# Kernel tuning notes

Hardware: AMD Instinct MI355X
Metric: run time of the kernel (lower is better)

Reference implementation:

```python
import math
import jax, jax.numpy as jnp
import numpy as np

B, T, D = 2, 1024, 512
H, DK = 8, 64


def setup_inputs() -> dict:
    key = jax.random.key(0)
    ks = jax.random.split(key, 7)
    s = 1.0 / math.sqrt(D)
    x = jax.random.normal(ks[0], (B, T, D), dtype=jnp.float32)
    Wq = jax.random.normal(ks[1], (D, H * DK), dtype=jnp.float32) * s
    Wk = jax.random.normal(ks[2], (D, H * DK), dtype=jnp.float32) * s
    Wv = jax.random.normal(ks[3], (D, H * DK), dtype=jnp.float32) * s
    Wo = jax.random.normal(ks[4], (H * DK, D), dtype=jnp.float32) * s
    Wg = jax.random.normal(ks[5], (D, H * DK), dtype=jnp.float32) * 0.02
    bg = jnp.ones((H * DK,), dtype=jnp.float32)  # gate_bias_init = 1.0
    return {"x": x, "Wq": Wq, "Wk": Wk, "Wv": Wv, "Wo": Wo, "Wg": Wg, "bg": bg}


def reference(x, Wq, Wk, Wv, Wo, Wg, bg):
    b, t, d = x.shape
    Q = jax.nn.relu(x @ Wq).reshape(b, t, H, DK)
    K = jax.nn.relu(x @ Wk).reshape(b, t, H, DK)
    V = (x @ Wv).reshape(b, t, H, DK)
    angle = jnp.arange(t, dtype=x.dtype) * (math.pi / (2 * t))  # (T,)
    cosw = jnp.cos(angle)[None, :, None, None]
    sinw = jnp.sin(angle)[None, :, None, None]
    Qc, Qs = Q * cosw, Q * sinw
    Kc, Ks = K * cosw, K * sinw
    # cumulative KV outer products: (B,T,H,DK,DK)
    Sc = jnp.cumsum(jnp.einsum('bthd,bthe->bthde', Kc, V), axis=1)
    Ss = jnp.cumsum(jnp.einsum('bthd,bthe->bthde', Ks, V), axis=1)
    o = jnp.einsum('bthd,bthde->bthe', Qc, Sc) + jnp.einsum('bthd,bthde->bthe', Qs, Ss)
    zc = jnp.cumsum(Kc, axis=1)
    zs = jnp.cumsum(Ks, axis=1)
    z = jnp.einsum('bthd,bthd->bth', Qc, zc) + jnp.einsum('bthd,bthd->bth', Qs, zs)
    z = jnp.maximum(z, 1e-6)[..., None]
    o = o / z
    gate = jax.nn.sigmoid((x @ Wg + bg).reshape(b, t, H, DK))
    o = o * gate
    return o.reshape(b, t, H * DK) @ Wo
```

## Files before the change

kernel.cpp:

```cpp
#include <hip/hip_runtime.h>
#include <math.h>

#define B_ 2
#define T_ 1024
#define D_ 512
#define H_ 8
#define DK_ 64
#define NBH_ 16
#define C_ 32
#define G_ 32

#define PI_OVER_2T 0.00153398078788564122971808758949f

typedef float f32x4 __attribute__((ext_vector_type(4)));
typedef short s16x8 __attribute__((ext_vector_type(8)));

__device__ __forceinline__ ushort f2bf(float x) {
    unsigned u = __float_as_uint(x);
    unsigned r = (u + 0x7fffu + ((u >> 16) & 1u)) >> 16;
    return (ushort)r;
}
__device__ __forceinline__ float bf2f(ushort u) {
    return __uint_as_float((unsigned)u << 16);
}

__device__ __forceinline__ void async16(void* lds, const void* g) {
    __builtin_amdgcn_global_load_lds(
        (const __attribute__((address_space(1))) void*)g,
        (__attribute__((address_space(3))) void*)lds, 16, 0, 0);
}

__global__ __launch_bounds__(256) void k_conv(
    const float* __restrict__ x,
    const float* __restrict__ Wq, const float* __restrict__ Wk,
    const float* __restrict__ Wv, const float* __restrict__ Wg,
    const float* __restrict__ Wo,
    ushort* __restrict__ xb, ushort* __restrict__ WtAll)
{
    __shared__ float Ts[64][65];
    const int bx = blockIdx.x;
    const int tid = threadIdx.x;
    if (bx < 1024) {
        int i = (bx * 256 + tid) * 4;
        float4 v = *(const float4*)&x[i];
        ushort4 o;
        o.x = f2bf(v.x); o.y = f2bf(v.y); o.z = f2bf(v.z); o.w = f2bf(v.w);
        *(ushort4*)&xb[i] = o;
        return;
    }
    const int bid = bx - 1024;
    const int mi = bid >> 6;
    const int t64 = bid & 63;
    const float* __restrict__ W = (mi == 0) ? Wq : (mi == 1) ? Wk
                                 : (mi == 2) ? Wv : (mi == 3) ? Wg : Wo;
    const int tr = t64 >> 3, tc = t64 & 7;
#pragma unroll
    for (int p = 0; p < 4; p++) {
        int row = p * 16 + (tid >> 4);
        int c4 = (tid & 15) * 4;
        float4 v = *(const float4*)&W[(size_t)(tr * 64 + row) * 512 + tc * 64 + c4];
        Ts[row][c4 + 0] = v.x; Ts[row][c4 + 1] = v.y;
        Ts[row][c4 + 2] = v.z; Ts[row][c4 + 3] = v.w;
    }
    __syncthreads();
    const int nl = tid >> 2, kc = (tid & 3) * 16;
    ushort buf[16];
#pragma unroll
    for (int u = 0; u < 16; u++) buf[u] = f2bf(Ts[kc + u][nl]);
    ushort* dst = WtAll + (size_t)mi * 262144 + (size_t)(tc * 64 + nl) * 512
                  + tr * 64 + kc;
    *(uint4*)dst = *(uint4*)&buf[0];
    *(uint4*)(dst + 8) = *(uint4*)&buf[8];
}

__global__ __launch_bounds__(256) void k_g0(
    const ushort* __restrict__ A, const ushort* __restrict__ WtAll,
    const float* __restrict__ bg,
    ushort* __restrict__ Qg, ushort* __restrict__ Kg,
    ushort* __restrict__ Vg, ushort* __restrict__ Gg,
    ushort* __restrict__ Sst, float* __restrict__ Zst)
{
    __shared__ union {
        struct { ushort As[2][64 * 64]; ushort Bs[2][2 * 64 * 64]; } s;
        struct { ushort KcT[64 * 72]; ushort KsT[64 * 72];
                 ushort VT[64 * 72]; ushort KR[64 * 72];
                 ushort VR[64 * 72]; } e;
    } sm;
    __shared__ float cosR[64], sinR[64];

    const int tid = threadIdx.x;
    const int ct = blockIdx.x;
    const int rowBase = blockIdx.y * 64;
    const bool isKV = (ct >= 8);
    const int matCol = (ct & 7) * 64;
    const ushort* __restrict__ B0 = WtAll + (size_t)(isKV ? 1 : 0) * 262144;
    const ushort* __restrict__ B1 = WtAll + (size_t)(isKV ? 2 : 3) * 262144;

    const int wave = tid >> 6, lane = tid & 63;
    const int q = lane >> 4, ln = lane & 15;
    const int mB = (wave >> 1) * 32, nB = (wave & 1) * 32;

    int fu[2];
    const ushort* gA[2];
    const ushort* gB0[2];
    const ushort* gB1[2];
#pragma unroll
    for (int u = 0; u < 2; u++) {
        int f = tid * 8 + u * 2048;
        int r = f >> 6;
        int gc = ((f >> 3) & 7) ^ (r & 7);
        fu[u] = f;
        gA[u]  = A  + (size_t)(rowBase + r) * 512 + gc * 8;
        gB0[u] = B0 + (size_t)(matCol + r) * 512 + gc * 8;
        gB1[u] = B1 + (size_t)(matCol + r) * 512 + gc * 8;
    }

    f32x4 accA[2][2], accB[2][2];
#pragma unroll
    for (int i = 0; i < 2; i++)
#pragma unroll
        for (int j = 0; j < 2; j++) {
            accA[i][j] = (f32x4){0.f, 0.f, 0.f, 0.f};
            accB[i][j] = (f32x4){0.f, 0.f, 0.f, 0.f};
        }

    int aoff[2][2], boff[2][2];
#pragma unroll
    for (int i = 0; i < 2; i++) {
        int ra = mB + i * 16 + ln;
#pragma unroll
        for (int ks = 0; ks < 2; ks++)
            aoff[i][ks] = ra * 64 + (((ks * 4 + q) ^ (ra & 7)) * 8);
    }
#pragma unroll
    for (int j = 0; j < 2; j++) {
        int rb = nB + j * 16 + ln;
#pragma unroll
        for (int ks = 0; ks < 2; ks++)
            boff[j][ks] = rb * 64 + (((ks * 4 + q) ^ (rb & 7)) * 8);
    }

#pragma unroll
    for (int u = 0; u < 2; u++) {
        async16(&sm.s.As[0][fu[u]], gA[u]);
        async16(&sm.s.Bs[0][fu[u]], gB0[u]);
        async16(&sm.s.Bs[0][4096 + fu[u]], gB1[u]);
    }

    int cur = 0;
    for (int kb = 0; kb < 512; kb += 64) {
        __syncthreads();
        if (kb + 64 < 512) {
            int nxt = cur ^ 1;
#pragma unroll
            for (int u = 0; u < 2; u++) {
                async16(&sm.s.As[nxt][fu[u]], gA[u] + kb + 64);
                async16(&sm.s.Bs[nxt][fu[u]], gB0[u] + kb + 64);
                async16(&sm.s.Bs[nxt][4096 + fu[u]], gB1[u] + kb + 64);
            }
        }
#pragma unroll
        for (int ks = 0; ks < 2; ks++) {
            s16x8 af[2], b0f[2], b1f[2];
#pragma unroll
            for (int i = 0; i < 2; i++)
                af[i] = *(const s16x8*)&sm.s.As[cur][aoff[i][ks]];
#pragma unroll
            for (int j = 0; j < 2; j++) {
                b0f[j] = *(const s16x8*)&sm.s.Bs[cur][boff[j][ks]];
                b1f[j] = *(const s16x8*)&sm.s.Bs[cur][4096 + boff[j][ks]];
            }
#pragma unroll
            for (int i = 0; i < 2; i++)
#pragma unroll
                for (int j = 0; j < 2; j++) {
                    accA[i][j] = __builtin_amdgcn_mfma_f32_16x16x32_bf16(
                        af[i], b0f[j], accA[i][j], 0, 0, 0);
                    accB[i][j] = __builtin_amdgcn_mfma_f32_16x16x32_bf16(
                        af[i], b1f[j], accB[i][j], 0, 0, 0);
                }
        }
        cur ^= 1;
    }
    if (isKV && tid < 64) {
        float a = (float)((rowBase + tid) & 1023) * PI_OVER_2T;
        cosR[tid] = cosf(a);
        sinR[tid] = sinf(a);
    }
    __syncthreads();

    if (!isKV) {
        ushort* QT = sm.e.KcT;
        ushort* GT = sm.e.KsT;
#pragma unroll
        for (int i = 0; i < 2; i++)
#pragma unroll
            for (int j = 0; j < 2; j++) {
                int colL = nB + j * 16 + ln;
                float bgv = bg[matCol + colL];
#pragma unroll
                for (int r = 0; r < 4; r++) {
                    int rowL = mB + i * 16 + q * 4 + r;
                    QT[rowL * 72 + colL] = f2bf(fmaxf(accA[i][j][r], 0.f));
                    GT[rowL * 72 + colL] =
                        f2bf(1.f / (1.f + expf(-(accB[i][j][r] + bgv))));
                }
            }
        __syncthreads();
#pragma unroll
        for (int it = 0; it < 2; it++) {
            int row = it * 32 + (tid >> 3), sub = tid & 7;
            uint4 qv = *(const uint4*)&QT[row * 72 + sub * 8];
            uint4 gv = *(const uint4*)&GT[row * 72 + sub * 8];
            size_t go = (size_t)(rowBase + row) * 512 + matCol + sub * 8;
            *(uint4*)&Qg[go] = qv;
            *(uint4*)&Gg[go] = gv;
        }
        return;
    }

    const int h = ct - 8;
    const int b = rowBase >> 10;
    const int c = wave >> 1;
    const int gG = ((rowBase & 1023) >> 5) + c;
    const int blk = (b * 8 + h) * 32 + gG;

    float zc[2] = {0.f, 0.f}, zs[2] = {0.f, 0.f};
#pragma unroll
    for (int i = 0; i < 2; i++)
#pragma unroll
        for (int r = 0; r < 4; r++) {
            int tLoc = mB + i * 16 + q * 4 + r;
            float ca = cosR[tLoc], sa = sinR[tLoc];
#pragma unroll
            for (int j = 0; j < 2; j++) {
                int col = nB + j * 16 + ln;
                float kv = fmaxf(accA[i][j][r], 0.f);
                float vv = accB[i][j][r];
                sm.e.KR[tLoc * 72 + col] = f2bf(kv);
                sm.e.VR[tLoc * 72 + col] = f2bf(vv);
                float kc = kv * ca, ks = kv * sa;
                sm.e.KcT[col * 72 + tLoc] = f2bf(kc);
                sm.e.KsT[col * 72 + tLoc] = f2bf(ks);
                sm.e.VT [col * 72 + tLoc] = f2bf(vv);
                zc[j] += kc; zs[j] += ks;
            }
        }
#pragma unroll
    for (int j = 0; j < 2; j++) {
        zc[j] += __shfl_xor(zc[j], 16); zc[j] += __shfl_xor(zc[j], 32);
        zs[j] += __shfl_xor(zs[j], 16); zs[j] += __shfl_xor(zs[j], 32);
    }
    if (q == 0) {
#pragma unroll
        for (int j = 0; j < 2; j++) {
            int d = nB + j * 16 + ln;
            Zst[(size_t)blk * 128 + d] = zc[j];
            Zst[(size_t)blk * 128 + 64 + d] = zs[j];
        }
    }
    __syncthreads();

#pragma unroll
    for (int it = 0; it < 2; it++) {
        int row = it * 32 + (tid >> 3), sub = tid & 7;
        uint4 kv4 = *(const uint4*)&sm.e.KR[row * 72 + sub * 8];
        uint4 vv4 = *(const uint4*)&sm.e.VR[row * 72 + sub * 8];
        size_t go = (size_t)(rowBase + row) * 512 + h * 64 + sub * 8;
        *(uint4*)&Kg[go] = kv4;
        *(uint4*)&Vg[go] = vv4;
    }

    {
        const int eh = (wave & 1) * 32;
        ushort* Sp = Sst + (size_t)blk * 8192;
        s16x8 av[2];
#pragma unroll
        for (int fi = 0; fi < 2; fi++)
            av[fi] = *(const s16x8*)&sm.e.VT[(eh + fi * 16 + ln) * 72
                                            + c * 32 + q * 8];
#pragma unroll
        for (int fj = 0; fj < 4; fj++) {
            s16x8 bc = *(const s16x8*)&sm.e.KcT[(fj * 16 + ln) * 72
                                                + c * 32 + q * 8];
            s16x8 bs = *(const s16x8*)&sm.e.KsT[(fj * 16 + ln) * 72
                                                + c * 32 + q * 8];
#pragma unroll
            for (int fi = 0; fi < 2; fi++) {
                f32x4 sc = __builtin_amdgcn_mfma_f32_16x16x32_bf16(
                    av[fi], bc, (f32x4){0.f, 0.f, 0.f, 0.f}, 0, 0, 0);
                f32x4 ss = __builtin_amdgcn_mfma_f32_16x16x32_bf16(
                    av[fi], bs, (f32x4){0.f, 0.f, 0.f, 0.f}, 0, 0, 0);
#pragma unroll
                for (int rr = 0; rr < 4; rr++) {
                    int e = eh + fi * 16 + q * 4 + rr;
                    int d = fj * 16 + ln;
                    Sp[e * 64 + d] = f2bf(sc[rr]);
                    Sp[4096 + e * 64 + d] = f2bf(ss[rr]);
                }
            }
        }
    }
}

template<int MODE, int TM, int TN, int BK>
__global__ __launch_bounds__(256) void k_gemm(
    const ushort* __restrict__ A, const ushort* __restrict__ Bt,
    const float* __restrict__ bg,
    void* __restrict__ O0v, void* __restrict__ O1v,
    void* __restrict__ O2v, void* __restrict__ O3v)
{
    constexpr int WM = TM / 2, WN = TN / 2;
    constexpr int FM = WM / 16, FN = WN / 16;
    constexpr int CH = BK / 8;
    constexpr int SH = (BK == 32) ? 1 : 0;
    constexpr int KS = BK / 32;
    constexpr int NA = TM * BK / 2048;
    constexpr int NB = TN * BK / 2048;
    static_assert(TM == 64 && TN == 32, "epilogue specialized");

    __shared__ ushort As[2][TM * BK];
    __shared__ ushort Bs[2][TN * BK];

    const int tid = threadIdx.x;
    const int ct = blockIdx.x;
    const int rowBase = blockIdx.y * TM;

    const int matCol = ct * TN;
    const ushort* __restrict__ Bmat = Bt;

    const int wave = tid >> 6, lane = tid & 63;
    const int q = lane >> 4, ln = lane & 15;
    const int mB = (wave >> 1) * WM, nB = (wave & 1) * WN;

    int fuA[NA], fuB[NB];
    const ushort* gA[NA];
    const ushort* gB[NB];
#pragma unroll
    for (int u = 0; u < NA; u++) {
        int fu = tid * 8 + u * 2048;
        int r = fu / BK;
        int slot = (fu >> 3) & (CH - 1);
        int gc = slot ^ ((r >> SH) & (CH - 1));
        fuA[u] = fu;
        gA[u] = A + (size_t)(rowBase + r) * 512 + gc * 8;
    }
#pragma unroll
    for (int u = 0; u < NB; u++) {
        int fu = tid * 8 + u * 2048;
        int r = fu / BK;
        int slot = (fu >> 3) & (CH - 1);
        int gc = slot ^ ((r >> SH) & (CH - 1));
        fuB[u] = fu;
        gB[u] = Bmat + (size_t)(matCol + r) * 512 + gc * 8;
    }

    f32x4 acc[FM][FN];
#pragma unroll
    for (int i = 0; i < FM; i++)
#pragma unroll
        for (int j = 0; j < FN; j++) acc[i][j] = (f32x4){0.f, 0.f, 0.f, 0.f};

    int aoff[FM][KS], boff[FN][KS];
#pragma unroll
    for (int i = 0; i < FM; i++) {
        int ra = mB + i * 16 + ln;
#pragma unroll
        for (int ks = 0; ks < KS; ks++)
            aoff[i][ks] = ra * BK + (((ks * 4 + q) ^ ((ra >> SH) & (CH - 1))) * 8);
    }
#pragma unroll
    for (int j = 0; j < FN; j++) {
        int rb = nB + j * 16 + ln;
#pragma unroll
        for (int ks = 0; ks < KS; ks++)
            boff[j][ks] = rb * BK + (((ks * 4 + q) ^ ((rb >> SH) & (CH - 1))) * 8);
    }

#pragma unroll
    for (int u = 0; u < NA; u++) async16(&As[0][fuA[u]], gA[u]);
#pragma unroll
    for (int u = 0; u < NB; u++) async16(&Bs[0][fuB[u]], gB[u]);

    int cur = 0;
    for (int kb = 0; kb < 512; kb += BK) {
        __syncthreads();
        if (kb + BK < 512) {
#pragma unroll
            for (int u = 0; u < NA; u++)
                async16(&As[cur ^ 1][fuA[u]], gA[u] + kb + BK);
#pragma unroll
            for (int u = 0; u < NB; u++)
                async16(&Bs[cur ^ 1][fuB[u]], gB[u] + kb + BK);
        }
#pragma unroll
        for (int ks = 0; ks < KS; ks++) {
            s16x8 af[FM], bf[FN];
#pragma unroll
            for (int i = 0; i < FM; i++)
                af[i] = *(const s16x8*)&As[cur][aoff[i][ks]];
#pragma unroll
            for (int j = 0; j < FN; j++)
                bf[j] = *(const s16x8*)&Bs[cur][boff[j][ks]];
#pragma unroll
            for (int i = 0; i < FM; i++)
#pragma unroll
                for (int j = 0; j < FN; j++)
                    acc[i][j] = __builtin_amdgcn_mfma_f32_16x16x32_bf16(
                        af[i], bf[j], acc[i][j], 0, 0, 0);
        }
        cur ^= 1;
    }
    __syncthreads();

    float* Ot = (float*)&As[0][0];
#pragma unroll
    for (int i = 0; i < FM; i++)
#pragma unroll
        for (int j = 0; j < FN; j++) {
            int colL = nB + j * 16 + ln;
#pragma unroll
            for (int r = 0; r < 4; r++) {
                int rowL = mB + i * 16 + q * 4 + r;
                Ot[rowL * 36 + colL] = acc[i][j][r];
            }
        }
    __syncthreads();

    float* __restrict__ Out = (float*)O0v;
    {
        int row = tid >> 2, sub = tid & 3;
        float4 a0 = *(const float4*)&Ot[row * 36 + sub * 8];
        float4 a1 = *(const float4*)&Ot[row * 36 + sub * 8 + 4];
        size_t go = (size_t)(rowBase + row) * 512 + matCol + sub * 8;
        *(float4*)&Out[go] = a0;
        *(float4*)&Out[go + 4] = a1;
    }
}

__global__ __launch_bounds__(256) void k_scan(
    ushort* __restrict__ Sst, float* __restrict__ Zst)
{
    int id = blockIdx.x * 256 + threadIdx.x;
    if (id < 32768) {
        int bh = id >> 11, i4 = (id & 2047) * 4;
        size_t base = (size_t)bh * (G_ * 8192) + i4;
        ushort4 v[G_];
#pragma unroll
        for (int g = 0; g < G_; g++)
            v[g] = *(const ushort4*)&Sst[base + (size_t)g * 8192];
        float rx = 0.f, ry = 0.f, rz = 0.f, rw = 0.f;
#pragma unroll
        for (int g = 0; g < G_; g++) {
            ushort4 t = v[g];
            ushort4 o;
            o.x = f2bf(rx); o.y = f2bf(ry); o.z = f2bf(rz); o.w = f2bf(rw);
            *(ushort4*)&Sst[base + (size_t)g * 8192] = o;
            rx += bf2f(t.x); ry += bf2f(t.y);
            rz += bf2f(t.z); rw += bf2f(t.w);
        }
    } else {
        int id2 = id - 32768;
        if (id2 >= 512) return;
        int bh = id2 >> 5, i4 = (id2 & 31) * 4;
        size_t base = (size_t)bh * (G_ * 128) + i4;
        float4 v[G_];
#pragma unroll
        for (int g = 0; g < G_; g++)
            v[g] = *(const float4*)&Zst[base + (size_t)g * 128];
        float4 run = make_float4(0.f, 0.f, 0.f, 0.f);
#pragma unroll
        for (int g = 0; g < G_; g++) {
            float4 t = v[g];
            *(float4*)&Zst[base + (size_t)g * 128] = run;
            run.x += t.x; run.y += t.y; run.z += t.z; run.w += t.w;
        }
    }
}

__global__ __launch_bounds__(256) void k_out_chunk(
    const ushort* __restrict__ Qg, const ushort* __restrict__ Kg,
    const ushort* __restrict__ Vg, const ushort* __restrict__ Gg,
    const ushort* __restrict__ Sst, const float* __restrict__ Zst,
    ushort* __restrict__ Op)
{
    __shared__ ushort VT[64 * 40];
    __shared__ ushort Pb[32 * 40];
    __shared__ float zinv[32];
    __shared__ float Ot[32 * 68];

    const int blk = blockIdx.x;
    const int bh = blk >> 5, g = blk & 31;
    const int b = bh >> 3, h = bh & 7;
    const int tid = threadIdx.x;
    const int rBase = b * T_ + g * C_;
    const int colB = h * DK_;
    const int wave = tid >> 6, lane = tid & 63;
    const int q = lane >> 4, ln = lane & 15;

    {
        int row = tid >> 3, c8 = (tid & 7) * 8;
        uint4 vraw = *(const uint4*)&Vg[(size_t)(rBase + row) * D_ + colB + c8];
        const ushort* vp = (const ushort*)&vraw;
#pragma unroll
        for (int u = 0; u < 8; u++) VT[(c8 + u) * 40 + row] = vp[u];
    }

    const int mi = wave >> 1, njp = wave & 1;
    const ushort* qrow = Qg + (size_t)(rBase + mi * 16 + ln) * D_ + colB;
    s16x8 aq0 = *(const s16x8*)&qrow[q * 8];
    s16x8 aq1 = *(const s16x8*)&qrow[32 + q * 8];
    {
        const ushort* krow = Kg + (size_t)(rBase + njp * 16 + ln) * D_ + colB;
        s16x8 bk0 = *(const s16x8*)&krow[q * 8];
        s16x8 bk1 = *(const s16x8*)&krow[32 + q * 8];
        f32x4 pacc = __builtin_amdgcn_mfma_f32_16x16x32_bf16(
            aq0, bk0, (f32x4){0.f, 0.f, 0.f, 0.f}, 0, 0, 0);
        pacc = __builtin_amdgcn_mfma_f32_16x16x32_bf16(aq1, bk1, pacc, 0, 0, 0);
        int sl = njp * 16 + ln;
#pragma unroll
        for (int r = 0; r < 4; r++) {
            int tl = mi * 16 + q * 4 + r;
            float w = (sl <= tl) ? cosf((float)(tl - sl) * PI_OVER_2T) : 0.f;
            Pb[tl * 40 + sl] = f2bf(pacc[r] * w);
        }
    }
    __syncthreads();

    {
        int t = tid >> 3, sub = tid & 7;
        uint4 qraw = *(const uint4*)&Qg[(size_t)(rBase + t) * D_ + colB + sub * 8];
        const ushort* qp = (const ushort*)&qraw;
        const float* zcp = Zst + (size_t)blk * 128 + sub * 8;
        float4 zc0 = *(const float4*)&zcp[0];
        float4 zc1 = *(const float4*)&zcp[4];
        float4 zs0 = *(const float4*)&zcp[64];
        float4 zs1 = *(const float4*)&zcp[68];
        float pc = 0.f, ps = 0.f;
        float zcv[8] = {zc0.x, zc0.y, zc0.z, zc0.w, zc1.x, zc1.y, zc1.z, zc1.w};
        float zsv[8] = {zs0.x, zs0.y, zs0.z, zs0.w, zs1.x, zs1.y, zs1.z, zs1.w};
#pragma unroll
        for (int u = 0; u < 8; u++) {
            float qf = bf2f(qp[u]);
            pc += qf * zcv[u]; ps += qf * zsv[u];
        }
        float pr = 0.f;
#pragma unroll
        for (int u = 0; u < 4; u++) pr += bf2f(Pb[t * 40 + sub * 4 + u]);
#pragma unroll
        for (int m = 1; m < 8; m <<= 1) {
            pc += __shfl_xor(pc, m);
            ps += __shfl_xor(ps, m);
            pr += __shfl_xor(pr, m);
        }
        if (sub == 0) {
            float at = (float)(g * C_ + t) * PI_OVER_2T;
            float z = cosf(at) * pc + sinf(at) * ps + pr;
            zinv[t] = 1.f / fmaxf(z, 1e-6f);
        }
    }
    __syncthreads();

    {
        float cr[4], sr[4];
#pragma unroll
        for (int r = 0; r < 4; r++) {
            int tl = mi * 16 + q * 4 + r;
            float at = (float)(g * C_ + tl) * PI_OVER_2T;
            cr[r] = cosf(at); sr[r] = sinf(at);
        }
        s16x8 pf = *(const s16x8*)&Pb[(mi * 16 + ln) * 40 + q * 8];
        const ushort* Sp = Sst + (size_t)blk * 8192;
#pragma unroll
        for (int jj = 0; jj < 2; jj++) {
            int nj = 2 * (wave & 1) + jj;
            const ushort* scp = Sp + (nj * 16 + ln) * 64;
            s16x8 bc0 = *(const s16x8*)&scp[q * 8];
            s16x8 bc1 = *(const s16x8*)&scp[32 + q * 8];
            s16x8 bs0 = *(const s16x8*)&scp[4096 + q * 8];
            s16x8 bs1 = *(const s16x8*)&scp[4096 + 32 + q * 8];
            s16x8 bv  = *(const s16x8*)&VT[(nj * 16 + ln) * 40 + q * 8];
            f32x4 accP = __builtin_amdgcn_mfma_f32_16x16x32_bf16(
                pf, bv, (f32x4){0.f, 0.f, 0.f, 0.f}, 0, 0, 0);
            f32x4 accC = __builtin_amdgcn_mfma_f32_16x16x32_bf16(
                aq0, bc0, (f32x4){0.f, 0.f, 0.f, 0.f}, 0, 0, 0);
            accC = __builtin_amdgcn_mfma_f32_16x16x32_bf16(aq1, bc1, accC, 0, 0, 0);
            f32x4 accS = __builtin_amdgcn_mfma_f32_16x16x32_bf16(
                aq0, bs0, (f32x4){0.f, 0.f, 0.f, 0.f}, 0, 0, 0);
            accS = __builtin_amdgcn_mfma_f32_16x16x32_bf16(aq1, bs1, accS, 0, 0, 0);
#pragma unroll
            for (int r = 0; r < 4; r++) {
                int tl = mi * 16 + q * 4 + r;
                Ot[tl * 68 + nj * 16 + ln] =
                    (accP[r] + cr[r] * accC[r] + sr[r] * accS[r]) * zinv[tl];
            }
        }
    }
    __syncthreads();

    {
        int t = tid >> 3, sub = tid & 7;
        size_t go = (size_t)(rBase + t) * D_ + colB + sub * 8;
        uint4 graw = *(const uint4*)&Gg[go];
        const ushort* gp = (const ushort*)&graw;
        const float* op = &Ot[t * 68 + sub * 8];
        ushort buf[8];
#pragma unroll
        for (int u = 0; u < 8; u++)
            buf[u] = f2bf(op[u] * bf2f(gp[u]));
        *(uint4*)&Op[go] = *(uint4*)&buf[0];
    }
}

extern "C" void kernel_launch(void* const* d_in, const int* in_sizes, int n_in,
                              void* d_out, int out_size, void* d_ws, size_t ws_size,
                              hipStream_t stream)
{
    const float* x  = (const float*)d_in[0];
    const float* Wq = (const float*)d_in[1];
    const float* Wk = (const float*)d_in[2];
    const float* Wv = (const float*)d_in[3];
    const float* Wo = (const float*)d_in[4];
    const float* Wg = (const float*)d_in[5];
    const float* bg = (const float*)d_in[6];
    float* out = (float*)d_out;

    ushort* wsu = (ushort*)d_ws;
    ushort* xb    = wsu;
    ushort* WtAll = xb + 1048576;
    ushort* Qg    = WtAll + 1310720;
    ushort* Kg    = Qg + 1048576;
    ushort* Vg    = Kg + 1048576;
    ushort* Gg    = Vg + 1048576;
    ushort* Sst   = Gg + 1048576;
    ushort* Opb   = Sst + 4194304;
    float*  Zst   = (float*)(Opb + 1048576);

    dim3 blk(256);
    k_conv<<<dim3(1344), blk, 0, stream>>>(x, Wq, Wk, Wv, Wg, Wo, xb, WtAll);
    k_g0<<<dim3(16, 32), blk, 0, stream>>>(
        xb, WtAll, bg, Qg, Kg, Vg, Gg, Sst, Zst);
    k_scan<<<dim3(130), blk, 0, stream>>>(Sst, Zst);
    k_out_chunk<<<dim3(NBH_ * G_), blk, 0, stream>>>(
        Qg, Kg, Vg, Gg, Sst, Zst, Opb);
    k_gemm<1, 64, 32, 64><<<dim3(16, 32), blk, 0, stream>>>(
        Opb, WtAll + (size_t)4 * 262144, nullptr,
        out, nullptr, nullptr, nullptr);
}
```

Before: 104.7 us.

## Fuse all stages into one cooperative megakernel with grid-wide syncs

Merges the conversion, QKV/gate projection, chunk-state scan, intra-chunk output and Wo GEMM kernels into a single cooperative kernel of 512 blocks, using grid.sync between phases. The aim is to remove the launch overhead and inter-kernel gaps of five separate launches. If the cooperative launch fails, it falls back to the original multi-kernel path. The trade-offs are the cost of grid-wide barriers, a fixed grid shape that limits parallelism in some phases (the scan uses only part of the grid), and LDS sized for the union of all phases, which may reduce occupancy.

After: 104.6 us. No clear change (-0.1%).

```diff
diff --git a/kernel.cpp b/kernel.cpp
--- a/kernel.cpp
+++ b/kernel.cpp
@@ -1,5 +1,8 @@
 #include <hip/hip_runtime.h>
+#include <hip/hip_cooperative_groups.h>
 #include <math.h>
+
+namespace cg = cooperative_groups;
 
 #define B_ 2
 #define T_ 1024
@@ -28,6 +31,551 @@
     __builtin_amdgcn_global_load_lds(
         (const __attribute__((address_space(1))) void*)g,
         (__attribute__((address_space(3))) void*)lds, 16, 0, 0);
+}
+
+__global__ __launch_bounds__(256, 2) void k_mega(
+    const float* __restrict__ x,
+    const float* __restrict__ Wq, const float* __restrict__ Wk,
+    const float* __restrict__ Wv, const float* __restrict__ Wg,
+    const float* __restrict__ Wo, const float* __restrict__ bg,
+    float* __restrict__ out, ushort* __restrict__ wsu)
+{
+    __shared__ union alignas(16) {
+        struct { float Ts[64 * 65]; } cv;
+        struct {
+            union {
+                struct { ushort As[2][4096]; ushort Bs[2][8192]; } s;
+                struct { ushort KcT[4608]; ushort KsT[4608];
+                         ushort VT[4608]; ushort KR[4608];
+                         ushort VR[4608]; } e;
+            } u;
+        } g0;
+        struct { ushort VT[2560]; ushort Pb[1280]; float zinv[32];
+                 float Ot[2176]; } oc;
+        struct { ushort As[2][4096]; ushort Bs[2][2048]; } gm;
+    } S;
+    __shared__ float cosR[64], sinR[64];
+
+    ushort* xb    = wsu;
+    ushort* WtAll = wsu + 1048576;
+    ushort* Qg    = WtAll + 1310720;
+    ushort* Kg    = Qg + 1048576;
+    ushort* Vg    = Kg + 1048576;
+    ushort* Gg    = Vg + 1048576;
+    ushort* Sst   = Gg + 1048576;
+    ushort* Opb   = Sst + 4194304;
+    float*  Zst   = (float*)(Opb + 1048576);
+    const ushort* WoT = WtAll + (size_t)4 * 262144;
+
+    const int tid  = threadIdx.x;
+    const int gbid = blockIdx.y * 16 + blockIdx.x;
+    const int wave = tid >> 6, lane = tid & 63;
+    const int q = lane >> 4, ln = lane & 15;
+
+    {
+        int gid = gbid * 256 + tid;
+#pragma unroll
+        for (int sgm = 0; sgm < 2; sgm++) {
+            int i = sgm * 524288 + gid * 4;
+            float4 v = *(const float4*)&x[i];
+            ushort4 o;
+            o.x = f2bf(v.x); o.y = f2bf(v.y); o.z = f2bf(v.z); o.w = f2bf(v.w);
+            *(ushort4*)&xb[i] = o;
+        }
+        if (gbid < 320) {
+            const int mi = gbid >> 6;
+            const int t64 = gbid & 63;
+            const float* __restrict__ W = (mi == 0) ? Wq : (mi == 1) ? Wk
+                                         : (mi == 2) ? Wv : (mi == 3) ? Wg : Wo;
+            const int tr = t64 >> 3, tc = t64 & 7;
+#pragma unroll
+            for (int p = 0; p < 4; p++) {
+                int row = p * 16 + (tid >> 4);
+                int c4 = (tid & 15) * 4;
+                float4 v = *(const float4*)
+                    &W[(size_t)(tr * 64 + row) * 512 + tc * 64 + c4];
+                S.cv.Ts[row * 65 + c4 + 0] = v.x;
+                S.cv.Ts[row * 65 + c4 + 1] = v.y;
+                S.cv.Ts[row * 65 + c4 + 2] = v.z;
+                S.cv.Ts[row * 65 + c4 + 3] = v.w;
+            }
+            __syncthreads();
+            const int nl = tid >> 2, kc = (tid & 3) * 16;
+            ushort buf[16];
+#pragma unroll
+            for (int u = 0; u < 16; u++) buf[u] = f2bf(S.cv.Ts[(kc + u) * 65 + nl]);
+            ushort* dst = WtAll + (size_t)mi * 262144
+                          + (size_t)(tc * 64 + nl) * 512 + tr * 64 + kc;
+            *(uint4*)dst = *(uint4*)&buf[0];
+            *(uint4*)(dst + 8) = *(uint4*)&buf[8];
+        }
+    }
+    __threadfence();
+    cg::this_grid().sync();
+
+    {
+        const int ct = blockIdx.x;
+        const int rowBase = blockIdx.y * 64;
+        const bool isKV = (ct >= 8);
+        const int matCol = (ct & 7) * 64;
+        const ushort* __restrict__ B0 = WtAll + (size_t)(isKV ? 1 : 0) * 262144;
+        const ushort* __restrict__ B1 = WtAll + (size_t)(isKV ? 2 : 3) * 262144;
+        const int mB = (wave >> 1) * 32, nB = (wave & 1) * 32;
+
+        int fu[2];
+        const ushort* gA[2];
+        const ushort* gB0[2];
+        const ushort* gB1[2];
+#pragma unroll
+        for (int u = 0; u < 2; u++) {
+            int f = tid * 8 + u * 2048;
+            int r = f >> 6;
+            int gc = ((f >> 3) & 7) ^ (r & 7);
+            fu[u] = f;
+            gA[u]  = xb + (size_t)(rowBase + r) * 512 + gc * 8;
+            gB0[u] = B0 + (size_t)(matCol + r) * 512 + gc * 8;
+            gB1[u] = B1 + (size_t)(matCol + r) * 512 + gc * 8;
+        }
+
+        f32x4 accA[2][2], accB[2][2];
+#pragma unroll
+        for (int i = 0; i < 2; i++)
+#pragma unroll
+            for (int j = 0; j < 2; j++) {
+                accA[i][j] = (f32x4){0.f, 0.f, 0.f, 0.f};
+                accB[i][j] = (f32x4){0.f, 0.f, 0.f, 0.f};
+            }
+
+        int aoff[2][2], boff[2][2];
+#pragma unroll
+        for (int i = 0; i < 2; i++) {
+            int ra = mB + i * 16 + ln;
+#pragma unroll
+            for (int ks = 0; ks < 2; ks++)
+                aoff[i][ks] = ra * 64 + (((ks * 4 + q) ^ (ra & 7)) * 8);
+        }
+#pragma unroll
+        for (int j = 0; j < 2; j++) {
+            int rb = nB + j * 16 + ln;
+#pragma unroll
+            for (int ks = 0; ks < 2; ks++)
+                boff[j][ks] = rb * 64 + (((ks * 4 + q) ^ (rb & 7)) * 8);
+        }
+
+#pragma unroll
+        for (int u = 0; u < 2; u++) {
+            async16(&S.g0.u.s.As[0][fu[u]], gA[u]);
+            async16(&S.g0.u.s.Bs[0][fu[u]], gB0[u]);
+            async16(&S.g0.u.s.Bs[0][4096 + fu[u]], gB1[u]);
+        }
+
+        int cur = 0;
+        for (int kb = 0; kb < 512; kb += 64) {
+            __syncthreads();
+            if (kb + 64 < 512) {
+                int nxt = cur ^ 1;
+#pragma unroll
+                for (int u = 0; u < 2; u++) {
+                    async16(&S.g0.u.s.As[nxt][fu[u]], gA[u] + kb + 64);
+                    async16(&S.g0.u.s.Bs[nxt][fu[u]], gB0[u] + kb + 64);
+                    async16(&S.g0.u.s.Bs[nxt][4096 + fu[u]], gB1[u] + kb + 64);
+                }
+            }
+#pragma unroll
+            for (int ks = 0; ks < 2; ks++) {
+                s16x8 af[2], b0f[2], b1f[2];
+#pragma unroll
+                for (int i = 0; i < 2; i++)
+                    af[i] = *(const s16x8*)&S.g0.u.s.As[cur][aoff[i][ks]];
+#pragma unroll
+                for (int j = 0; j < 2; j++) {
+                    b0f[j] = *(const s16x8*)&S.g0.u.s.Bs[cur][boff[j][ks]];
+                    b1f[j] = *(const s16x8*)&S.g0.u.s.Bs[cur][4096 + boff[j][ks]];
+                }
+#pragma unroll
+                for (int i = 0; i < 2; i++)
+#pragma unroll
+                    for (int j = 0; j < 2; j++) {
+                        accA[i][j] = __builtin_amdgcn_mfma_f32_16x16x32_bf16(
+                            af[i], b0f[j], accA[i][j], 0, 0, 0);
+                        accB[i][j] = __builtin_amdgcn_mfma_f32_16x16x32_bf16(
+                            af[i], b1f[j], accB[i][j], 0, 0, 0);
+                    }
+            }
+            cur ^= 1;
+        }
+        if (isKV && tid < 64) {
+            float a = (float)((rowBase + tid) & 1023) * PI_OVER_2T;
+            cosR[tid] = cosf(a);
+            sinR[tid] = sinf(a);
+        }
+        __syncthreads();
+
+        if (!isKV) {
+            ushort* QT = S.g0.u.e.KcT;
+            ushort* GT = S.g0.u.e.KsT;
+#pragma unroll
+            for (int i = 0; i < 2; i++)
+#pragma unroll
+                for (int j = 0; j < 2; j++) {
+                    int colL = nB + j * 16 + ln;
+                    float bgv = bg[matCol + colL];
+#pragma unroll
+                    for (int r = 0; r < 4; r++) {
+                        int rowL = mB + i * 16 + q * 4 + r;
+                        QT[rowL * 72 + colL] = f2bf(fmaxf(accA[i][j][r], 0.f));
+                        GT[rowL * 72 + colL] =
+                            f2bf(1.f / (1.f + expf(-(accB[i][j][r] + bgv))));
+                    }
+                }
+            __syncthreads();
+#pragma unroll
+            for (int it = 0; it < 2; it++) {
+                int row = it * 32 + (tid >> 3), sub = tid & 7;
+                uint4 qv = *(const uint4*)&QT[row * 72 + sub * 8];
+                uint4 gv = *(const uint4*)&GT[row * 72 + sub * 8];
+                size_t go = (size_t)(rowBase + row) * 512 + matCol + sub * 8;
+                *(uint4*)&Qg[go] = qv;
+                *(uint4*)&Gg[go] = gv;
+            }
+        } else {
+            const int h = ct - 8;
+            const int b = rowBase >> 10;
+            const int c = wave >> 1;
+            const int gG = ((rowBase & 1023) >> 5) + c;
+            const int blk = (b * 8 + h) * 32 + gG;
+
+            float zc[2] = {0.f, 0.f}, zs[2] = {0.f, 0.f};
+#pragma unroll
+            for (int i = 0; i < 2; i++)
+#pragma unroll
+                for (int r = 0; r < 4; r++) {
+                    int tLoc = mB + i * 16 + q * 4 + r;
+                    float ca = cosR[tLoc], sa = sinR[tLoc];
+#pragma unroll
+                    for (int j = 0; j < 2; j++) {
+                        int col = nB + j * 16 + ln;
+                        float kv = fmaxf(accA[i][j][r], 0.f);
+                        float vv = accB[i][j][r];
+                        S.g0.u.e.KR[tLoc * 72 + col] = f2bf(kv);
+                        S.g0.u.e.VR[tLoc * 72 + col] = f2bf(vv);
+                        float kc = kv * ca, ks = kv * sa;
+                        S.g0.u.e.KcT[col * 72 + tLoc] = f2bf(kc);
+                        S.g0.u.e.KsT[col * 72 + tLoc] = f2bf(ks);
+                        S.g0.u.e.VT [col * 72 + tLoc] = f2bf(vv);
+                        zc[j] += kc; zs[j] += ks;
+                    }
+                }
+#pragma unroll
+            for (int j = 0; j < 2; j++) {
+                zc[j] += __shfl_xor(zc[j], 16); zc[j] += __shfl_xor(zc[j], 32);
+                zs[j] += __shfl_xor(zs[j], 16); zs[j] += __shfl_xor(zs[j], 32);
+            }
+            if (q == 0) {
+#pragma unroll
+                for (int j = 0; j < 2; j++) {
+                    int d = nB + j * 16 + ln;
+                    Zst[(size_t)blk * 128 + d] = zc[j];
+                    Zst[(size_t)blk * 128 + 64 + d] = zs[j];
+                }
+            }
+            __syncthreads();
+
+#pragma unroll
+            for (int it = 0; it < 2; it++) {
+                int row = it * 32 + (tid >> 3), sub = tid & 7;
+                uint4 kv4 = *(const uint4*)&S.g0.u.e.KR[row * 72 + sub * 8];
+                uint4 vv4 = *(const uint4*)&S.g0.u.e.VR[row * 72 + sub * 8];
+                size_t go = (size_t)(rowBase + row) * 512 + h * 64 + sub * 8;
+                *(uint4*)&Kg[go] = kv4;
+                *(uint4*)&Vg[go] = vv4;
+            }
+
+            {
+                const int eh = (wave & 1) * 32;
+                ushort* Sp = Sst + (size_t)blk * 8192;
+                s16x8 av[2];
+#pragma unroll
+                for (int fi = 0; fi < 2; fi++)
+                    av[fi] = *(const s16x8*)&S.g0.u.e.VT[(eh + fi * 16 + ln) * 72
+                                                         + c * 32 + q * 8];
+#pragma unroll
+                for (int fj = 0; fj < 4; fj++) {
+                    s16x8 bc = *(const s16x8*)&S.g0.u.e.KcT[(fj * 16 + ln) * 72
+                                                            + c * 32 + q * 8];
+                    s16x8 bs = *(const s16x8*)&S.g0.u.e.KsT[(fj * 16 + ln) * 72
+                                                            + c * 32 + q * 8];
+#pragma unroll
+                    for (int fi = 0; fi < 2; fi++) {
+                        f32x4 sc = __builtin_amdgcn_mfma_f32_16x16x32_bf16(
+                            av[fi], bc, (f32x4){0.f, 0.f, 0.f, 0.f}, 0, 0, 0);
+                        f32x4 ss = __builtin_amdgcn_mfma_f32_16x16x32_bf16(
+                            av[fi], bs, (f32x4){0.f, 0.f, 0.f, 0.f}, 0, 0, 0);
+#pragma unroll
+                        for (int rr = 0; rr < 4; rr++) {
+                            int e = eh + fi * 16 + q * 4 + rr;
+                            int d = fj * 16 + ln;
+                            Sp[e * 64 + d] = f2bf(sc[rr]);
+                            Sp[4096 + e * 64 + d] = f2bf(ss[rr]);
+                        }
+                    }
+                }
+            }
+        }
+    }
+    __threadfence();
+    cg::this_grid().sync();
+
+    {
+        int id = gbid * 256 + tid;
+        if (id < 32768) {
+            int bh = id >> 11, i4 = (id & 2047) * 4;
+            size_t base = (size_t)bh * (G_ * 8192) + i4;
+            ushort4 v[G_];
+#pragma unroll
+            for (int g = 0; g < G_; g++)
+                v[g] = *(const ushort4*)&Sst[base + (size_t)g * 8192];
+            float rx = 0.f, ry = 0.f, rz = 0.f, rw = 0.f;
+#pragma unroll
+            for (int g = 0; g < G_; g++) {
+                ushort4 t = v[g];
+                ushort4 o;
+                o.x = f2bf(rx); o.y = f2bf(ry); o.z = f2bf(rz); o.w = f2bf(rw);
+                *(ushort4*)&Sst[base + (size_t)g * 8192] = o;
+                rx += bf2f(t.x); ry += bf2f(t.y);
+                rz += bf2f(t.z); rw += bf2f(t.w);
+            }
+        } else if (id < 33280) {
+            int id2 = id - 32768;
+            int bh = id2 >> 5, i4 = (id2 & 31) * 4;
+            size_t base = (size_t)bh * (G_ * 128) + i4;
+            float4 v[G_];
+#pragma unroll
+            for (int g = 0; g < G_; g++)
+                v[g] = *(const float4*)&Zst[base + (size_t)g * 128];
+            float4 run = make_float4(0.f, 0.f, 0.f, 0.f);
+#pragma unroll
+            for (int g = 0; g < G_; g++) {
+                float4 t = v[g];
+                *(float4*)&Zst[base + (size_t)g * 128] = run;
+                run.x += t.x; run.y += t.y; run.z += t.z; run.w += t.w;
+            }
+        }
+    }
+    __threadfence();
+    cg::this_grid().sync();
+
+    {
+        const int blk = gbid;
+        const int bh = blk >> 5, g = blk & 31;
+        const int b = bh >> 3, h = bh & 7;
+        const int rBase = b * T_ + g * C_;
+        const int colB = h * DK_;
+
+        {
+            int row = tid >> 3, c8 = (tid & 7) * 8;
+            uint4 vraw = *(const uint4*)&Vg[(size_t)(rBase + row) * D_ + colB + c8];
+            const ushort* vp = (const ushort*)&vraw;
+#pragma unroll
+            for (int u = 0; u < 8; u++) S.oc.VT[(c8 + u) * 40 + row] = vp[u];
+        }
+
+        const int mi = wave >> 1, njp = wave & 1;
+        const ushort* qrow = Qg + (size_t)(rBase + mi * 16 + ln) * D_ + colB;
+        s16x8 aq0 = *(const s16x8*)&qrow[q * 8];
+        s16x8 aq1 = *(const s16x8*)&qrow[32 + q * 8];
+        {
+            const ushort* krow = Kg + (size_t)(rBase + njp * 16 + ln) * D_ + colB;
+            s16x8 bk0 = *(const s16x8*)&krow[q * 8];
+            s16x8 bk1 = *(const s16x8*)&krow[32 + q * 8];
+            f32x4 pacc = __builtin_amdgcn_mfma_f32_16x16x32_bf16(
+                aq0, bk0, (f32x4){0.f, 0.f, 0.f, 0.f}, 0, 0, 0);
+            pacc = __builtin_amdgcn_mfma_f32_16x16x32_bf16(aq1, bk1, pacc, 0, 0, 0);
+            int sl = njp * 16 + ln;
+#pragma unroll
+            for (int r = 0; r < 4; r++) {
+                int tl = mi * 16 + q * 4 + r;
+                float w = (sl <= tl) ? cosf((float)(tl - sl) * PI_OVER_2T) : 0.f;
+                S.oc.Pb[tl * 40 + sl] = f2bf(pacc[r] * w);
+            }
+        }
+        __syncthreads();
+
+        {
+            int t = tid >> 3, sub = tid & 7;
+            uint4 qraw = *(const uint4*)&Qg[(size_t)(rBase + t) * D_ + colB + sub * 8];
+            const ushort* qp = (const ushort*)&qraw;
+            const float* zcp = Zst + (size_t)blk * 128 + sub * 8;
+            float4 zc0 = *(const float4*)&zcp[0];
+            float4 zc1 = *(const float4*)&zcp[4];
+            float4 zs0 = *(const float4*)&zcp[64];
+            float4 zs1 = *(const float4*)&zcp[68];
+            float pc = 0.f, ps = 0.f;
+            float zcv[8] = {zc0.x, zc0.y, zc0.z, zc0.w, zc1.x, zc1.y, zc1.z, zc1.w};
+            float zsv[8] = {zs0.x, zs0.y, zs0.z, zs0.w, zs1.x, zs1.y, zs1.z, zs1.w};
+#pragma unroll
+            for (int u = 0; u < 8; u++) {
+                float qf = bf2f(qp[u]);
+                pc += qf * zcv[u]; ps += qf * zsv[u];
+            }
+            float pr = 0.f;
+#pragma unroll
+            for (int u = 0; u < 4; u++) pr += bf2f(S.oc.Pb[t * 40 + sub * 4 + u]);
+#pragma unroll
+            for (int m = 1; m < 8; m <<= 1) {
+                pc += __shfl_xor(pc, m);
+                ps += __shfl_xor(ps, m);
+                pr += __shfl_xor(pr, m);
+            }
+            if (sub == 0) {
+                float at = (float)(g * C_ + t) * PI_OVER_2T;
+                float z = cosf(at) * pc + sinf(at) * ps + pr;
+                S.oc.zinv[t] = 1.f / fmaxf(z, 1e-6f);
+            }
+        }
+        __syncthreads();
+
+        {
+            float cr[4], sr[4];
+#pragma unroll
+            for (int r = 0; r < 4; r++) {
+                int tl = mi * 16 + q * 4 + r;
+                float at = (float)(g * C_ + tl) * PI_OVER_2T;
+                cr[r] = cosf(at); sr[r] = sinf(at);
+            }
+            s16x8 pf = *(const s16x8*)&S.oc.Pb[(mi * 16 + ln) * 40 + q * 8];
+            const ushort* Sp = Sst + (size_t)blk * 8192;
+#pragma unroll
+            for (int jj = 0; jj < 2; jj++) {
+                int nj = 2 * (wave & 1) + jj;
+                const ushort* scp = Sp + (nj * 16 + ln) * 64;
+                s16x8 bc0 = *(const s16x8*)&scp[q * 8];
+                s16x8 bc1 = *(const s16x8*)&scp[32 + q * 8];
+                s16x8 bs0 = *(const s16x8*)&scp[4096 + q * 8];
+                s16x8 bs1 = *(const s16x8*)&scp[4096 + 32 + q * 8];
+                s16x8 bv  = *(const s16x8*)&S.oc.VT[(nj * 16 + ln) * 40 + q * 8];
+                f32x4 accP = __builtin_amdgcn_mfma_f32_16x16x32_bf16(
+                    pf, bv, (f32x4){0.f, 0.f, 0.f, 0.f}, 0, 0, 0);
+                f32x4 accC = __builtin_amdgcn_mfma_f32_16x16x32_bf16(
+                    aq0, bc0, (f32x4){0.f, 0.f, 0.f, 0.f}, 0, 0, 0);
+                accC = __builtin_amdgcn_mfma_f32_16x16x32_bf16(aq1, bc1, accC, 0, 0, 0);
+                f32x4 accS = __builtin_amdgcn_mfma_f32_16x16x32_bf16(
+                    aq0, bs0, (f32x4){0.f, 0.f, 0.f, 0.f}, 0, 0, 0);
+                accS = __builtin_amdgcn_mfma_f32_16x16x32_bf16(aq1, bs1, accS, 0, 0, 0);
+#pragma unroll
+                for (int r = 0; r < 4; r++) {
+                    int tl = mi * 16 + q * 4 + r;
+                    S.oc.Ot[tl * 68 + nj * 16 + ln] =
+                        (accP[r] + cr[r] * accC[r] + sr[r] * accS[r]) * S.oc.zinv[tl];
+                }
+            }
+        }
+        __syncthreads();
+
+        {
+            int t = tid >> 3, sub = tid & 7;
+            size_t go = (size_t)(rBase + t) * D_ + colB + sub * 8;
+            uint4 graw = *(const uint4*)&Gg[go];
+            const ushort* gp = (const ushort*)&graw;
+            const float* op = &S.oc.Ot[t * 68 + sub * 8];
+            ushort buf[8];
+#pragma unroll
+            for (int u = 0; u < 8; u++)
+                buf[u] = f2bf(op[u] * bf2f(gp[u]));
+            *(uint4*)&Opb[go] = *(uint4*)&buf[0];
+        }
+    }
+    __threadfence();
+    cg::this_grid().sync();
+
+    {
+        const int ct4 = blockIdx.x;
+        const int rowB4 = blockIdx.y * 64;
+        const int matCol4 = ct4 * 32;
+        const int mB4 = (wave >> 1) * 32, nB4 = (wave & 1) * 16;
+
+        int fuA4[2];
+        const ushort* gA4[2];
+#pragma unroll
+        for (int u = 0; u < 2; u++) {
+            int f = tid * 8 + u * 2048;
+            int r = f >> 6;
+            int gc = ((f >> 3) & 7) ^ (r & 7);
+            fuA4[u] = f;
+            gA4[u] = Opb + (size_t)(rowB4 + r) * 512 + gc * 8;
+        }
+        int fuB4;
+        const ushort* gB4;
+        {
+            int f = tid * 8;
+            int r = f >> 6;
+            int gc = ((f >> 3) & 7) ^ (r & 7);
+            fuB4 = f;
+            gB4 = WoT + (size_t)(matCol4 + r) * 512 + gc * 8;
+        }
+
+        f32x4 acc4[2];
+        acc4[0] = (f32x4){0.f, 0.f, 0.f, 0.f};
+        acc4[1] = (f32x4){0.f, 0.f, 0.f, 0.f};
+        int aoff4[2][2], boff4[2];
+#pragma unroll
+        for (int i = 0; i < 2; i++) {
+            int ra = mB4 + i * 16 + ln;
+#pragma unroll
+            for (int ks = 0; ks < 2; ks++)
+                aoff4[i][ks] = ra * 64 + (((ks * 4 + q) ^ (ra & 7)) * 8);
+        }
+        {
+            int rb = nB4 + ln;
+#pragma unroll
+            for (int ks = 0; ks < 2; ks++)
+                boff4[ks] = rb * 64 + (((ks * 4 + q) ^ (rb & 7)) * 8);
+        }
+
+#pragma unroll
+        for (int u = 0; u < 2; u++) async16(&S.gm.As[0][fuA4[u]], gA4[u]);
+        async16(&S.gm.Bs[0][fuB4], gB4);
+
+        int cur = 0;
+        for (int kb = 0; kb < 512; kb += 64) {
+            __syncthreads();
+            if (kb + 64 < 512) {
+#pragma unroll
+                for (int u = 0; u < 2; u++)
+                    async16(&S.gm.As[cur ^ 1][fuA4[u]], gA4[u] + kb + 64);
+                async16(&S.gm.Bs[cur ^ 1][fuB4], gB4 + kb + 64);
+            }
+#pragma unroll
+            for (int ks = 0; ks < 2; ks++) {
+                s16x8 af0 = *(const s16x8*)&S.gm.As[cur][aoff4[0][ks]];
+                s16x8 af1 = *(const s16x8*)&S.gm.As[cur][aoff4[1][ks]];
+                s16x8 bf  = *(const s16x8*)&S.gm.Bs[cur][boff4[ks]];
+                acc4[0] = __builtin_amdgcn_mfma_f32_16x16x32_bf16(
+                    af0, bf, acc4[0], 0, 0, 0);
+                acc4[1] = __builtin_amdgcn_mfma_f32_16x16x32_bf16(
+                    af1, bf, acc4[1], 0, 0, 0);
+            }
+            cur ^= 1;
+        }
+        __syncthreads();
+
+        float* Ot4 = (float*)&S.gm.As[0][0];
+#pragma unroll
+        for (int i = 0; i < 2; i++)
+#pragma unroll
+            for (int r = 0; r < 4; r++)
+                Ot4[(mB4 + i * 16 + q * 4 + r) * 36 + nB4 + ln] = acc4[i][r];
+        __syncthreads();
+
+        {
+            int row = tid >> 2, sub = tid & 3;
+            float4 a0 = *(const float4*)&Ot4[row * 36 + sub * 8];
+            float4 a1 = *(const float4*)&Ot4[row * 36 + sub * 8 + 4];
+            size_t go = (size_t)(rowB4 + row) * 512 + matCol4 + sub * 8;
+            *(float4*)&out[go] = a0;
+            *(float4*)&out[go + 4] = a1;
+        }
+    }
 }
 
 __global__ __launch_bounds__(256) void k_conv(
@@ -624,8 +1172,22 @@
     const float* Wg = (const float*)d_in[5];
     const float* bg = (const float*)d_in[6];
     float* out = (float*)d_out;
-
     ushort* wsu = (ushort*)d_ws;
+
+    static int mode = -1;
+
+    if (mode != 0) {
+        void* args[] = {
+            (void*)&x, (void*)&Wq, (void*)&Wk, (void*)&Wv, (void*)&Wg,
+            (void*)&Wo, (void*)&bg, (void*)&out, (void*)&wsu
+        };
+        hipError_t e = hipLaunchCooperativeKernel(
+            (const void*)k_mega, dim3(16, 32), dim3(256, 1, 1), args, 0, stream);
+        if (mode == -1) mode = (e == hipSuccess) ? 1 : 0;
+        if (mode == 1) return;
+        (void)hipGetLastError();
+    }
+
     ushort* xb    = wsu;
     ushort* WtAll = xb + 1048576;
     ushort* Qg    = WtAll + 1310720;
```
